# Kernel optimization log

Measured on AMD Instinct MI355X. Metric: run time of the kernel, lower is better.

The kernel has to match this reference:

```python
import jax, jax.numpy as jnp
import numpy as np

N = 100000   # nodes
E = 1600000  # edges
G = 512      # graphs
EPS_MSG = 1e-7   # GENConv message eps
EPS_SM = 1e-16   # PyG softmax denom eps
BN_EPS = 1e-5    # BatchNorm eps (eval mode, running mean=0, var=1)


def setup_inputs() -> dict:
    key = jax.random.key(0)
    ks = iter(jax.random.split(key, 40))
    d = {}
    d['x'] = jax.random.normal(next(ks), (N, 10), dtype=jnp.float32)
    d['edge_index'] = jax.random.randint(next(ks), (2, E), 0, N, dtype=jnp.int64)
    d['batch'] = jax.random.randint(next(ks), (N,), 0, G, dtype=jnp.int64)

    def lin(k, fo, fi):
        k1, k2 = jax.random.split(k)
        s = 1.0 / np.sqrt(fi)
        return (jax.random.uniform(k1, (fo, fi), jnp.float32, -s, s),
                jax.random.uniform(k2, (fo,), jnp.float32, -s, s))

    # conv1: lin_src/lin_dst 10->100, MLP [100,200,100] with BN(200)
    d['c1_src_w'], d['c1_src_b'] = lin(next(ks), 100, 10)
    d['c1_dst_w'], d['c1_dst_b'] = lin(next(ks), 100, 10)
    d['c1_w1'], d['c1_b1'] = lin(next(ks), 200, 100)
    d['c1_g'] = jnp.ones((200,), jnp.float32)
    d['c1_be'] = jnp.zeros((200,), jnp.float32)
    d['c1_w2'], d['c1_b2'] = lin(next(ks), 100, 200)
    # conv2 / conv3: in==out -> no lin_src/dst; MLP [100,200,100]
    for p in ('c2', 'c3'):
        d[p + '_w1'], d[p + '_b1'] = lin(next(ks), 200, 100)
        d[p + '_g'] = jnp.ones((200,), jnp.float32)
        d[p + '_be'] = jnp.zeros((200,), jnp.float32)
        d[p + '_w2'], d[p + '_b2'] = lin(next(ks), 100, 200)
    d['fc1_w'], d['fc1_b'] = lin(next(ks), 100, 200)
    d['cls_w'], d['cls_b'] = lin(next(ks), 2, 100)
    return d


def _genconv(x, src, dst, src_w, src_b, dst_w, dst_b, w1, b1, g, be, w2, b2):
    # GENConv, aggr='softmax', t=1, eval-mode BN in MLP
    h = x if src_w is None else x @ src_w.T + src_b          # [N, 100]
    msg = jax.nn.relu(h[src]) + EPS_MSG                       # [E, 100]
    m = jax.ops.segment_max(msg, dst, num_segments=N)
    m = jnp.where(jnp.isfinite(m), m, 0.0)
    e = jnp.exp(msg - m[dst])
    den = jax.ops.segment_sum(e, dst, num_segments=N)
    alpha = e / (den[dst] + EPS_SM)
    agg = jax.ops.segment_sum(alpha * msg, dst, num_segments=N)  # [N, 100]
    xd = x if dst_w is None else x @ dst_w.T + dst_b
    out = agg + xd
    # MLP: Linear -> BN(eval: mean0,var1) -> ReLU -> Linear
    hh = out @ w1.T + b1
    hh = hh * (g / np.sqrt(1.0 + BN_EPS)) + be
    hh = jax.nn.relu(hh)
    return hh @ w2.T + b2


def _readout(x, batch):
    s = jax.ops.segment_sum(x, batch, num_segments=G)
    cnt = jax.ops.segment_sum(jnp.ones((x.shape[0],), x.dtype), batch, num_segments=G)
    mean = s / jnp.maximum(cnt, 1.0)[:, None]
    mx = jax.ops.segment_max(x, batch, num_segments=G)
    mx = jnp.where(jnp.isfinite(mx), mx, 0.0)
    return jnp.concatenate([mean, mx], axis=-1)  # [G, 200]


def reference(x, edge_index, batch,
              c1_src_w, c1_src_b, c1_dst_w, c1_dst_b, c1_w1, c1_b1, c1_g, c1_be, c1_w2, c1_b2,
              c2_w1, c2_b1, c2_g, c2_be, c2_w2, c2_b2,
              c3_w1, c3_b1, c3_g, c3_be, c3_w2, c3_b2,
              fc1_w, fc1_b, cls_w, cls_b):
    src, dst = edge_index[0], edge_index[1]
    h = jax.nn.relu(_genconv(x, src, dst, c1_src_w, c1_src_b, c1_dst_w, c1_dst_b,
                             c1_w1, c1_b1, c1_g, c1_be, c1_w2, c1_b2))
    x1 = _readout(h, batch)
    h = jax.nn.relu(_genconv(h, src, dst, None, None, None, None,
                             c2_w1, c2_b1, c2_g, c2_be, c2_w2, c2_b2))
    x2 = _readout(h, batch)
    h = jax.nn.relu(_genconv(h, src, dst, None, None, None, None,
                             c3_w1, c3_b1, c3_g, c3_be, c3_w2, c3_b2))
    x3 = _readout(h, batch)
    encode = jax.nn.relu(x1) + jax.nn.relu(x2) + jax.nn.relu(x3)  # [G, 200]
    z = jax.nn.relu(encode @ fc1_w.T + fc1_b)  # dropout is identity in eval
    logits = z @ cls_w.T + cls_b               # [G, 2]
    return (logits, encode)
```

## Files before the change

### kernel.cpp

```cpp
#include <hip/hip_runtime.h>
#include <cstdint>
#include <cstddef>

#define XF 10
#define NF 100
#define HF 200
#define BSHIFT 8
#define NBLK_G 512
#define MAXBK 512
#define RCH 4

typedef _Float16 f16x8 __attribute__((ext_vector_type(8)));
typedef _Float16 h2 __attribute__((ext_vector_type(2)));
typedef float f32x4 __attribute__((ext_vector_type(4)));

static __device__ __forceinline__ float bn_scale(float g) {
    return g * 0.9999950000374997f;
}

__global__ __launch_bounds__(256) void csr_count_kernel(const int* __restrict__ eidx,
                                                        int* __restrict__ bmat,
                                                        int E, int nbk, int epb) {
    __shared__ int hist[MAXBK];
    for (int j = threadIdx.x; j < nbk; j += 256) hist[j] = 0;
    __syncthreads();
    int base = blockIdx.x * epb;
    int end = base + epb; if (end > E) end = E;
    for (int e = base + threadIdx.x; e < end; e += 256) {
        int d = eidx[E + e];
        atomicAdd(&hist[d >> BSHIFT], 1);
    }
    __syncthreads();
    for (int j = threadIdx.x; j < nbk; j += 256)
        bmat[(size_t)j * NBLK_G + blockIdx.x] = hist[j];
}

__global__ __launch_bounds__(256) void scan1x_kernel(int* __restrict__ a,
                                                     int* __restrict__ blocksum, int n) {
    __shared__ int s[256];
    int t = threadIdx.x;
    int base = blockIdx.x * 1024 + t * 4;
    int v[4]; int tot = 0;
#pragma unroll
    for (int i = 0; i < 4; ++i) {
        v[i] = (base + i < n) ? a[base + i] : 0;
        tot += v[i];
    }
    s[t] = tot;
    __syncthreads();
    for (int off = 1; off < 256; off <<= 1) {
        int add = (t >= off) ? s[t - off] : 0;
        __syncthreads();
        s[t] += add;
        __syncthreads();
    }
    int run = s[t] - tot;
#pragma unroll
    for (int i = 0; i < 4; ++i) {
        if (base + i < n) a[base + i] = run;
        run += v[i];
    }
    if (t == 255) blocksum[blockIdx.x] = s[255];
}

__global__ void small_scan_kernel(const int* __restrict__ in, int in_stride,
                                  int* __restrict__ cur, int cur_stride,
                                  int* __restrict__ indptr, int n) {
    __shared__ int s[256];
    int t = threadIdx.x;
    int base = t * 4;
    int v[4]; int tot = 0;
#pragma unroll
    for (int i = 0; i < 4; ++i) {
        v[i] = (base + i < n) ? in[(base + i) * in_stride] : 0;
        tot += v[i];
    }
    s[t] = tot;
    __syncthreads();
    for (int off = 1; off < 256; off <<= 1) {
        int add = (t >= off) ? s[t - off] : 0;
        __syncthreads();
        s[t] += add;
        __syncthreads();
    }
    int run = s[t] - tot;
#pragma unroll
    for (int i = 0; i < 4; ++i) {
        if (base + i < n) {
            cur[(base + i) * cur_stride] = run;
            run += v[i];
            if (indptr) indptr[base + i + 1] = run;
        }
    }
    if (t == 0 && indptr) indptr[0] = 0;
}

__global__ __launch_bounds__(256) void csr_scatter_kernel(const int* __restrict__ eidx,
                                                          const int* __restrict__ bmat,
                                                          const int* __restrict__ blocksum,
                                                          int* __restrict__ packed,
                                                          int E, int nbk, int epb) {
    __shared__ int cur[MAXBK];
    for (int j = threadIdx.x; j < nbk; j += 256) {
        size_t idx = (size_t)j * NBLK_G + blockIdx.x;
        cur[j] = bmat[idx] + blocksum[idx >> 10];
    }
    __syncthreads();
    int base = blockIdx.x * epb;
    int end = base + epb; if (end > E) end = E;
    for (int e = base + threadIdx.x; e < end; e += 256) {
        int s = eidx[e];
        int d = eidx[E + e];
        int p = atomicAdd(&cur[d >> BSHIFT], 1);
        packed[p] = s | ((d & 255) << 24);
    }
}

__global__ __launch_bounds__(256) void csr_finalize_kernel(const int* __restrict__ bmat,
                                                           const int* __restrict__ blocksum,
                                                           const int* __restrict__ packed,
                                                           int* __restrict__ indptr,
                                                           int* __restrict__ esrc,
                                                           int E, int nbk, int n) {
    __shared__ int cnt[256];
    __shared__ int s[256];
    __shared__ int cur[256];
    int b = blockIdx.x;
    int t = threadIdx.x;
    size_t i0 = (size_t)b * NBLK_G;
    int ebeg = bmat[i0] + blocksum[i0 >> 10];
    int eend = E;
    if (b + 1 < nbk) {
        size_t i1 = (size_t)(b + 1) * NBLK_G;
        eend = bmat[i1] + blocksum[i1 >> 10];
    }
    cnt[t] = 0;
    __syncthreads();
    for (int i = ebeg + t; i < eend; i += 256)
        atomicAdd(&cnt[((unsigned)packed[i]) >> 24], 1);
    __syncthreads();
    int tot = cnt[t];
    s[t] = tot;
    __syncthreads();
    for (int off = 1; off < 256; off <<= 1) {
        int add = (t >= off) ? s[t - off] : 0;
        __syncthreads();
        s[t] += add;
        __syncthreads();
    }
    int off_ex = s[t] - tot;
    int node = (b << BSHIFT) + t;
    if (node < n) indptr[node] = ebeg + off_ex;
    if (b == nbk - 1 && t == 0) indptr[n] = E;
    cur[t] = ebeg + off_ex;
    __syncthreads();
    for (int i = ebeg + t; i < eend; i += 256) {
        int p = packed[i];
        int pos = atomicAdd(&cur[((unsigned)p) >> 24], 1);
        esrc[pos] = p & 0xFFFFFF;
    }
}

__global__ __launch_bounds__(256) void gcnt_kernel(const int* __restrict__ batch,
                                                   int* __restrict__ gcount, int n) {
    int i = blockIdx.x * 256 + threadIdx.x;
    if (i < n) atomicAdd(&gcount[batch[i]], 1);
}

__global__ __launch_bounds__(256) void gfill_kernel(const int* __restrict__ batch,
                                                    int* __restrict__ gcur,
                                                    int* __restrict__ gnodes, int n) {
    int i = blockIdx.x * 256 + threadIdx.x;
    if (i >= n) return;
    int g = batch[i];
    int p = atomicAdd(&gcur[g], 1);
    gnodes[p] = i;
}

struct WArgs {
    const float* src[6];
    _Float16* dst[6];
};
__global__ __launch_bounds__(256) void wconv_kernel(WArgs wa) {
    int w = blockIdx.y;
    int idx = blockIdx.x * 256 + threadIdx.x;
    int J, K, j, k;
    if (w < 3) { J = 200; K = 100; j = idx >> 7; k = idx & 127; }
    else       { J = 100; K = 200; j = idx >> 8; k = idx & 255; }
    float v = (j < J && k < K) ? wa.src[w][j * K + k] : 0.f;
    wa.dst[w][idx] = (_Float16)v;
}

__global__ __launch_bounds__(256) void lin10_kernel(const float* __restrict__ x,
                                                    const float* __restrict__ sw,
                                                    const float* __restrict__ sb,
                                                    const float* __restrict__ dw,
                                                    const float* __restrict__ db,
                                                    _Float16* __restrict__ h16,
                                                    _Float16* __restrict__ xd16, int n_nodes) {
    int t = threadIdx.x;
    int slot = t >> 6, lane = t & 63;
    bool act = lane < 50;
    int f0 = 2 * lane, f1 = f0 + 1;
    float ws0[XF], ws1[XF], wd0[XF], wd1[XF];
    float bs0 = 0.f, bs1 = 0.f, bd0 = 0.f, bd1 = 0.f;
    if (act) {
#pragma unroll
        for (int k = 0; k < XF; ++k) {
            ws0[k] = sw[f0 * XF + k]; ws1[k] = sw[f1 * XF + k];
            wd0[k] = dw[f0 * XF + k]; wd1[k] = dw[f1 * XF + k];
        }
        bs0 = sb[f0]; bs1 = sb[f1]; bd0 = db[f0]; bd1 = db[f1];
    }
    for (int it = 0; it < 16; ++it) {
        int n = blockIdx.x * 64 + it * 4 + slot;
        if (n >= n_nodes) continue;
        float a0 = bs0, a1 = bs1, b0 = bd0, b1 = bd1;
        if (act) {
            const float2* xp = (const float2*)(x + (size_t)n * XF);
            float xv[XF];
#pragma unroll
            for (int k = 0; k < 5; ++k) { float2 v = xp[k]; xv[2 * k] = v.x; xv[2 * k + 1] = v.y; }
#pragma unroll
            for (int k = 0; k < XF; ++k) {
                a0 = fmaf(xv[k], ws0[k], a0);
                a1 = fmaf(xv[k], ws1[k], a1);
                b0 = fmaf(xv[k], wd0[k], b0);
                b1 = fmaf(xv[k], wd1[k], b1);
            }
        } else { a0 = a1 = b0 = b1 = 0.f; }
        ((h2*)(h16 + (size_t)n * 128))[lane] = (h2){(_Float16)a0, (_Float16)a1};
        ((h2*)(xd16 + (size_t)n * 128))[lane] = (h2){(_Float16)b0, (_Float16)b1};
    }
}

__global__ __launch_bounds__(128) void agg_kernel(const _Float16* __restrict__ h16,
                                                  const _Float16* __restrict__ xd16,
                                                  const int* __restrict__ indptr,
                                                  const int* __restrict__ esrc,
                                                  _Float16* __restrict__ c16, int n_nodes) {
    int n = blockIdx.x * 2 + (threadIdx.x >> 6);
    if (n >= n_nodes) return;
    int lane = threadIdx.x & 63;
    int ln = (lane < 50) ? lane : 0;
    int beg = __builtin_amdgcn_readfirstlane(indptr[n]);
    int end = __builtin_amdgcn_readfirstlane(indptr[n + 1]);
    int deg = end - beg;
    const h2* hb = (const h2*)h16;
    float d0 = 0.f, d1 = 0.f, s0 = 0.f, s1 = 0.f;
    const float L2E = 1.44269504088896f;
    h2 va[8], vb[8];
    if (deg > 0) {
#pragma unroll
        for (int k = 0; k < 8; ++k) {
            int j = (k < deg) ? k : deg - 1;
            unsigned sidx = (unsigned)esrc[beg + j];
            va[k] = hb[(size_t)sidx * 64 + ln];
        }
    }
    for (int r = 0; r < deg; r += 8) {
        if (r + 8 < deg) {
#pragma unroll
            for (int k = 0; k < 8; ++k) {
                int j = (r + 8 + k < deg) ? r + 8 + k : deg - 1;
                unsigned sidx = (unsigned)esrc[beg + j];
                vb[k] = hb[(size_t)sidx * 64 + ln];
            }
        }
        int km = deg - r; if (km > 8) km = 8;
#pragma unroll
        for (int k = 0; k < 8; ++k) {
            if (k < km) {
                float a0 = fmaxf((float)va[k].x, 0.f) + 1e-7f;
                float a1 = fmaxf((float)va[k].y, 0.f) + 1e-7f;
                float e0 = __builtin_amdgcn_exp2f(fmaf(a0, L2E, -40.f));
                float e1 = __builtin_amdgcn_exp2f(fmaf(a1, L2E, -40.f));
                d0 += e0; s0 = fmaf(e0, a0, s0);
                d1 += e1; s1 = fmaf(e1, a1, s1);
            }
        }
#pragma unroll
        for (int k = 0; k < 8; ++k) va[k] = vb[k];
    }
    const float EPS = 9.094947e-29f;
    float g0 = s0 / (d0 + EPS);
    float g1 = s1 / (d1 + EPS);
    float o0 = 0.f, o1 = 0.f;
    if (lane < 50) {
        h2 xv = ((const h2*)(xd16 + (size_t)n * 128))[lane];
        o0 = g0 + (float)xv.x;
        o1 = g1 + (float)xv.y;
    }
    ((h2*)(c16 + (size_t)n * 128))[lane] = (h2){(_Float16)o0, (_Float16)o1};
}

__global__ __launch_bounds__(256, 3) void mlp_fused_kernel(const _Float16* __restrict__ A,
                                                           const _Float16* __restrict__ W1,
                                                           const float* __restrict__ b1v,
                                                           const float* __restrict__ g1v,
                                                           const float* __restrict__ be1v,
                                                           const _Float16* __restrict__ W2,
                                                           const float* __restrict__ b2v,
                                                           _Float16* __restrict__ out16,
                                                           int M) {
    __shared__ _Float16 hh[64][264];
    int wave = threadIdx.x >> 6;
    int lane = threadIdx.x & 63;
    int l15 = lane & 15, quad = lane >> 4;
    long m0 = (long)blockIdx.x * 64;

    const _Float16* aptr = A + (m0 + l15) * 128 + quad * 8;
    const _Float16* w1p  = W1 + (size_t)(wave * 64 + l15) * 128 + quad * 8;
    f32x4 acc[4][4] = {};
#pragma unroll 2
    for (int ks = 0; ks < 4; ++ks) {
        f16x8 bfr[4], afr[4];
#pragma unroll
        for (int ct = 0; ct < 4; ++ct) bfr[ct] = *(const f16x8*)(w1p + (size_t)ct * 16 * 128 + ks * 32);
#pragma unroll
        for (int i = 0; i < 4; ++i) afr[i] = *(const f16x8*)(aptr + (size_t)i * 16 * 128 + ks * 32);
#pragma unroll
        for (int i = 0; i < 4; ++i)
#pragma unroll
            for (int ct = 0; ct < 4; ++ct)
                acc[i][ct] = __builtin_amdgcn_mfma_f32_16x16x32_f16(afr[i], bfr[ct], acc[i][ct], 0, 0, 0);
    }
#pragma unroll
    for (int ct = 0; ct < 4; ++ct) {
        int col = wave * 64 + ct * 16 + l15;
        bool cv = col < HF;
        float bi = cv ? b1v[col] : 0.f;
        float gm = cv ? bn_scale(g1v[col]) : 0.f;
        float bt = cv ? be1v[col] : 0.f;
#pragma unroll
        for (int i = 0; i < 4; ++i)
#pragma unroll
            for (int r = 0; r < 4; ++r) {
                float v = fmaxf((acc[i][ct][r] + bi) * gm + bt, 0.f);
                hh[i * 16 + quad * 4 + r][col] = (_Float16)v;
            }
    }
    __syncthreads();

    const _Float16* w2p = W2 + (size_t)(wave * 32 + l15) * 256 + quad * 8;
    f32x4 o[4][2] = {};
#pragma unroll 2
    for (int ks = 0; ks < 8; ++ks) {
        f16x8 bfr[2], afr[4];
#pragma unroll
        for (int ct = 0; ct < 2; ++ct) bfr[ct] = *(const f16x8*)(w2p + (size_t)ct * 16 * 256 + ks * 32);
#pragma unroll
        for (int i = 0; i < 4; ++i) afr[i] = *(const f16x8*)(&hh[i * 16 + l15][quad * 8 + ks * 32]);
#pragma unroll
        for (int i = 0; i < 4; ++i)
#pragma unroll
            for (int ct = 0; ct < 2; ++ct)
                o[i][ct] = __builtin_amdgcn_mfma_f32_16x16x32_f16(afr[i], bfr[ct], o[i][ct], 0, 0, 0);
    }
#pragma unroll
    for (int ct = 0; ct < 2; ++ct) {
        int col = wave * 32 + ct * 16 + l15;
        bool cv = col < NF;
        float bi = cv ? b2v[col] : 0.f;
#pragma unroll
        for (int i = 0; i < 4; ++i)
#pragma unroll
            for (int r = 0; r < 4; ++r) {
                long row = m0 + i * 16 + quad * 4 + r;
                float v = fmaxf(o[i][ct][r] + bi, 0.f);
                if (!cv) v = 0.f;
                if (row < M) out16[row * 128 + col] = (_Float16)v;
            }
    }
}

__global__ __launch_bounds__(256) void readout2_kernel(const _Float16* __restrict__ h16,
                                                       const int* __restrict__ gindptr,
                                                       const int* __restrict__ gnodes,
                                                       float* __restrict__ sumpart,
                                                       float* __restrict__ maxpart, int G) {
    __shared__ float ls[4][128];
    __shared__ float lm[4][128];
    int g = blockIdx.x, ch = blockIdx.y;
    int wave = threadIdx.x >> 6;
    int lane = threadIdx.x & 63;
    int ln = (lane < 50) ? lane : 0;
    int beg = gindptr[g], end = gindptr[g + 1];
    const h2* hb = (const h2*)h16;
    float s0 = 0.f, s1 = 0.f, m0 = 0.f, m1 = 0.f;
    int i = beg + ch * 4 + wave;
    int nd = (i < end) ? gnodes[i] : 0;
    for (; i < end; i += 16) {
        int ndn = (i + 16 < end) ? gnodes[i + 16] : 0;
        h2 v = hb[(size_t)nd * 64 + ln];
        float v0 = (float)v.x, v1 = (float)v.y;
        s0 += v0; s1 += v1;
        m0 = fmaxf(m0, v0); m1 = fmaxf(m1, v1);
        nd = ndn;
    }
    ls[wave][2 * lane] = s0; ls[wave][2 * lane + 1] = s1;
    lm[wave][2 * lane] = m0; lm[wave][2 * lane + 1] = m1;
    __syncthreads();
    int f = threadIdx.x;
    if (f < NF) {
        float ss = ls[0][f] + ls[1][f] + ls[2][f] + ls[3][f];
        float mm = fmaxf(fmaxf(lm[0][f], lm[1][f]), fmaxf(lm[2][f], lm[3][f]));
        sumpart[((size_t)ch * G + g) * NF + f] = ss;
        maxpart[((size_t)ch * G + g) * NF + f] = mm;
    }
}

__global__ __launch_bounds__(256) void head_kernel(const float* __restrict__ rbuf,
                                                   const int* __restrict__ gindptr,
                                                   const float* __restrict__ fc1w,
                                                   const float* __restrict__ fc1b,
                                                   const float* __restrict__ clsw,
                                                   const float* __restrict__ clsb,
                                                   float* __restrict__ out, int G) {
    __shared__ float enc[HF];
    __shared__ float z[NF];
    int g = blockIdx.x;
    int t = threadIdx.x;
    float ic = 1.f / fmaxf((float)(gindptr[g + 1] - gindptr[g]), 1.f);
    if (t < HF) {
        float e = 0.f;
        if (t < NF) {
#pragma unroll
            for (int l = 0; l < 3; ++l) {
                float s = 0.f;
#pragma unroll
                for (int ch = 0; ch < RCH; ++ch)
                    s += rbuf[(((size_t)(l * 2) * RCH + ch) * G + g) * NF + t];
                e += fmaxf(s * ic, 0.f);
            }
        } else {
            int f = t - NF;
#pragma unroll
            for (int l = 0; l < 3; ++l) {
                float mm = 0.f;
#pragma unroll
                for (int ch = 0; ch < RCH; ++ch)
                    mm = fmaxf(mm, rbuf[(((size_t)(l * 2 + 1) * RCH + ch) * G + g) * NF + f]);
                e += fmaxf(mm, 0.f);
            }
        }
        enc[t] = e;
        out[G * 2 + (size_t)g * HF + t] = e;
    }
    __syncthreads();
    if (t < NF) {
        float a = fc1b[t];
        for (int k = 0; k < HF; ++k) a += enc[k] * fc1w[t * HF + k];
        z[t] = fmaxf(a, 0.f);
    }
    __syncthreads();
    if (t < 2) {
        float a = clsb[t];
        for (int k = 0; k < NF; ++k) a += z[k] * clsw[t * NF + k];
        out[(size_t)g * 2 + t] = a;
    }
}

extern "C" void kernel_launch(void* const* d_in, const int* in_sizes, int n_in,
                              void* d_out, int out_size, void* d_ws, size_t ws_size,
                              hipStream_t stream) {
    const float* x        = (const float*)d_in[0];
    const int*   eidx     = (const int*)d_in[1];
    const int*   batch    = (const int*)d_in[2];
    const float* c1_src_w = (const float*)d_in[3];
    const float* c1_src_b = (const float*)d_in[4];
    const float* c1_dst_w = (const float*)d_in[5];
    const float* c1_dst_b = (const float*)d_in[6];
    const float* cw1[3] = {(const float*)d_in[7],  (const float*)d_in[13], (const float*)d_in[19]};
    const float* cb1[3] = {(const float*)d_in[8],  (const float*)d_in[14], (const float*)d_in[20]};
    const float* cg[3]  = {(const float*)d_in[9],  (const float*)d_in[15], (const float*)d_in[21]};
    const float* cbe[3] = {(const float*)d_in[10], (const float*)d_in[16], (const float*)d_in[22]};
    const float* cw2[3] = {(const float*)d_in[11], (const float*)d_in[17], (const float*)d_in[23]};
    const float* cb2[3] = {(const float*)d_in[12], (const float*)d_in[18], (const float*)d_in[24]};
    const float* fc1w = (const float*)d_in[25];
    const float* fc1b = (const float*)d_in[26];
    const float* clsw = (const float*)d_in[27];
    const float* clsb = (const float*)d_in[28];

    const int N = in_sizes[0] / XF;
    const int E = in_sizes[1] / 2;
    const int G = out_size / 202;
    const int Mpad = (N + 63) & ~63;
    const int NBK = (N + 255) >> BSHIFT;
    const int EPB = (E + NBLK_G - 1) / NBLK_G;
    const int BM = NBK * NBLK_G;
    const int NB2 = (BM + 1023) / 1024;

    char* p = (char*)d_ws;
    auto alloc = [&](size_t bytes) {
        char* r = p;
        p += (bytes + 255) & ~(size_t)255;
        return r;
    };
    _Float16* h16  = (_Float16*)alloc((size_t)Mpad * 128 * 2);
    _Float16* C16  = (_Float16*)alloc((size_t)Mpad * 128 * 2);
    _Float16* xd16 = (_Float16*)alloc((size_t)Mpad * 128 * 2);
    _Float16* W16  = (_Float16*)alloc((size_t)6 * 32768 * 2);
    int* packed   = (int*)alloc((size_t)E * 4);
    int* esrc     = (int*)alloc((size_t)E * 4);
    int* indptr   = (int*)alloc((size_t)(N + 1) * 4);
    int* bmat     = (int*)alloc((size_t)BM * 4);
    int* blocksum = (int*)alloc((size_t)NB2 * 4);
    int* gcount   = (int*)alloc((size_t)G * 4);
    int* gcur     = (int*)alloc((size_t)G * 4);
    int* gindptr  = (int*)alloc((size_t)(G + 1) * 4);
    int* gnodes   = (int*)alloc((size_t)N * 4);
    float* rbuf   = (float*)alloc((size_t)6 * RCH * G * NF * 4);

    (void)hipMemsetAsync(gcount, 0, (size_t)G * 4, stream);

    csr_count_kernel<<<NBLK_G, 256, 0, stream>>>(eidx, bmat, E, NBK, EPB);
    scan1x_kernel<<<NB2, 256, 0, stream>>>(bmat, blocksum, BM);
    small_scan_kernel<<<1, 256, 0, stream>>>(blocksum, 1, blocksum, 1, nullptr, NB2);
    csr_scatter_kernel<<<NBLK_G, 256, 0, stream>>>(eidx, bmat, blocksum, packed, E, NBK, EPB);
    csr_finalize_kernel<<<NBK, 256, 0, stream>>>(bmat, blocksum, packed, indptr, esrc, E, NBK, N);

    gcnt_kernel<<<(N + 255) / 256, 256, 0, stream>>>(batch, gcount, N);
    small_scan_kernel<<<1, 256, 0, stream>>>(gcount, 1, gcur, 1, gindptr, G);
    gfill_kernel<<<(N + 255) / 256, 256, 0, stream>>>(batch, gcur, gnodes, N);

    WArgs wa;
    for (int l = 0; l < 3; ++l) {
        wa.src[l] = cw1[l];     wa.dst[l] = W16 + (size_t)l * 32768;
        wa.src[3 + l] = cw2[l]; wa.dst[3 + l] = W16 + (size_t)(3 + l) * 32768;
    }
    wconv_kernel<<<dim3(128, 6), 256, 0, stream>>>(wa);

    lin10_kernel<<<(N + 63) / 64, 256, 0, stream>>>(x, c1_src_w, c1_src_b,
                                                    c1_dst_w, c1_dst_b, h16, xd16, N);

    for (int l = 0; l < 3; ++l) {
        const _Float16* xdp = (l == 0) ? xd16 : h16;
        agg_kernel<<<(N + 1) / 2, 128, 0, stream>>>(h16, xdp, indptr, esrc, C16, N);
        mlp_fused_kernel<<<Mpad / 64, 256, 0, stream>>>(
            C16, W16 + (size_t)l * 32768, cb1[l], cg[l], cbe[l],
            W16 + (size_t)(3 + l) * 32768, cb2[l], h16, N);
        readout2_kernel<<<dim3(G, RCH), 256, 0, stream>>>(
            h16, gindptr, gnodes,
            rbuf + (size_t)(l * 2) * RCH * G * NF,
            rbuf + (size_t)(l * 2 + 1) * RCH * G * NF, G);
    }

    head_kernel<<<G, 256, 0, stream>>>(rbuf, gindptr, fc1w, fc1b, clsw, clsb, (float*)d_out, G);
    (void)ws_size;
}
```

Before: 635.3 us.

## Split each node's edge aggregation across two waves and skip redundant ReLU

The aggregation kernel now gives each destination node two wavefronts, each handling alternating edges, and merges their partial softmax sums through shared memory before the final divide and residual add. This doubles the memory-level parallelism per node for the gather-heavy edge loop, which has an average degree of 16. A template flag also drops the ReLU in layers 2 and 3, whose inputs already passed through a ReLU. The cost is a block-wide barrier and an LDS exchange, plus a second wave sitting idle during the finalize step.

New measurement: 865.2 us. 36.2% more time.

```diff
diff --git a/kernel.cpp b/kernel.cpp
--- a/kernel.cpp
+++ b/kernel.cpp
@@ -234,64 +234,79 @@
     }
 }
 
-__global__ __launch_bounds__(128) void agg_kernel(const _Float16* __restrict__ h16,
+template <bool RELU>
+__global__ __launch_bounds__(256) void agg_kernel(const _Float16* __restrict__ h16,
                                                   const _Float16* __restrict__ xd16,
                                                   const int* __restrict__ indptr,
                                                   const int* __restrict__ esrc,
                                                   _Float16* __restrict__ c16, int n_nodes) {
-    int n = blockIdx.x * 2 + (threadIdx.x >> 6);
-    if (n >= n_nodes) return;
+    __shared__ float4 part[4][64];
+    int wave = threadIdx.x >> 6;
     int lane = threadIdx.x & 63;
+    int half = wave & 1;
+    int n = blockIdx.x * 2 + (wave >> 1);
     int ln = (lane < 50) ? lane : 0;
-    int beg = __builtin_amdgcn_readfirstlane(indptr[n]);
-    int end = __builtin_amdgcn_readfirstlane(indptr[n + 1]);
-    int deg = end - beg;
     const h2* hb = (const h2*)h16;
+    const float L2E = 1.44269504088896f;
     float d0 = 0.f, d1 = 0.f, s0 = 0.f, s1 = 0.f;
-    const float L2E = 1.44269504088896f;
-    h2 va[8], vb[8];
-    if (deg > 0) {
-#pragma unroll
-        for (int k = 0; k < 8; ++k) {
-            int j = (k < deg) ? k : deg - 1;
-            unsigned sidx = (unsigned)esrc[beg + j];
-            va[k] = hb[(size_t)sidx * 64 + ln];
+    if (n < n_nodes) {
+        int beg = __builtin_amdgcn_readfirstlane(indptr[n]);
+        int end = __builtin_amdgcn_readfirstlane(indptr[n + 1]);
+        int deg = end - beg;
+        int cnt = (deg - half + 1) >> 1;
+        if (cnt > 0) {
+            int base = beg + half;
+            h2 va[8], vb[8];
+#pragma unroll
+            for (int k = 0; k < 8; ++k) {
+                int j = (k < cnt) ? k : cnt - 1;
+                unsigned sidx = (unsigned)esrc[base + 2 * j];
+                va[k] = hb[(size_t)sidx * 64 + ln];
+            }
+            for (int r = 0; r < cnt; r += 8) {
+                if (r + 8 < cnt) {
+#pragma unroll
+                    for (int k = 0; k < 8; ++k) {
+                        int j = (r + 8 + k < cnt) ? r + 8 + k : cnt - 1;
+                        unsigned sidx = (unsigned)esrc[base + 2 * j];
+                        vb[k] = hb[(size_t)sidx * 64 + ln];
+                    }
+                }
+                int km = cnt - r; if (km > 8) km = 8;
+#pragma unroll
+                for (int k = 0; k < 8; ++k) {
+                    if (k < km) {
+                        float a0 = (float)va[k].x;
+                        float a1 = (float)va[k].y;
+                        if (RELU) { a0 = fmaxf(a0, 0.f); a1 = fmaxf(a1, 0.f); }
+                        a0 += 1e-7f; a1 += 1e-7f;
+                        float e0 = __builtin_amdgcn_exp2f(fmaf(a0, L2E, -40.f));
+                        float e1 = __builtin_amdgcn_exp2f(fmaf(a1, L2E, -40.f));
+                        d0 += e0; s0 = fmaf(e0, a0, s0);
+                        d1 += e1; s1 = fmaf(e1, a1, s1);
+                    }
+                }
+#pragma unroll
+                for (int k = 0; k < 8; ++k) va[k] = vb[k];
+            }
         }
     }
-    for (int r = 0; r < deg; r += 8) {
-        if (r + 8 < deg) {
-#pragma unroll
-            for (int k = 0; k < 8; ++k) {
-                int j = (r + 8 + k < deg) ? r + 8 + k : deg - 1;
-                unsigned sidx = (unsigned)esrc[beg + j];
-                vb[k] = hb[(size_t)sidx * 64 + ln];
-            }
+    part[wave][lane] = make_float4(d0, d1, s0, s1);
+    __syncthreads();
+    if (half == 0 && n < n_nodes) {
+        float4 o = part[wave | 1][lane];
+        d0 += o.x; d1 += o.y; s0 += o.z; s1 += o.w;
+        const float EPS = 9.094947e-29f;
+        float g0 = s0 / (d0 + EPS);
+        float g1 = s1 / (d1 + EPS);
+        float o0 = 0.f, o1 = 0.f;
+        if (lane < 50) {
+            h2 xv = ((const h2*)(xd16 + (size_t)n * 128))[lane];
+            o0 = g0 + (float)xv.x;
+            o1 = g1 + (float)xv.y;
         }
-        int km = deg - r; if (km > 8) km = 8;
-#pragma unroll
-        for (int k = 0; k < 8; ++k) {
-            if (k < km) {
-                float a0 = fmaxf((float)va[k].x, 0.f) + 1e-7f;
-                float a1 = fmaxf((float)va[k].y, 0.f) + 1e-7f;
-                float e0 = __builtin_amdgcn_exp2f(fmaf(a0, L2E, -40.f));
-                float e1 = __builtin_amdgcn_exp2f(fmaf(a1, L2E, -40.f));
-                d0 += e0; s0 = fmaf(e0, a0, s0);
-                d1 += e1; s1 = fmaf(e1, a1, s1);
-            }
-        }
-#pragma unroll
-        for (int k = 0; k < 8; ++k) va[k] = vb[k];
-    }
-    const float EPS = 9.094947e-29f;
-    float g0 = s0 / (d0 + EPS);
-    float g1 = s1 / (d1 + EPS);
-    float o0 = 0.f, o1 = 0.f;
-    if (lane < 50) {
-        h2 xv = ((const h2*)(xd16 + (size_t)n * 128))[lane];
-        o0 = g0 + (float)xv.x;
-        o1 = g1 + (float)xv.y;
-    }
-    ((h2*)(c16 + (size_t)n * 128))[lane] = (h2){(_Float16)o0, (_Float16)o1};
+        ((h2*)(c16 + (size_t)n * 128))[lane] = (h2){(_Float16)o0, (_Float16)o1};
+    }
 }
 
 __global__ __launch_bounds__(256, 3) void mlp_fused_kernel(const _Float16* __restrict__ A,
@@ -536,7 +551,10 @@
 
     for (int l = 0; l < 3; ++l) {
         const _Float16* xdp = (l == 0) ? xd16 : h16;
-        agg_kernel<<<(N + 1) / 2, 128, 0, stream>>>(h16, xdp, indptr, esrc, C16, N);
+        if (l == 0)
+            agg_kernel<true><<<(N + 1) / 2, 256, 0, stream>>>(h16, xdp, indptr, esrc, C16, N);
+        else
+            agg_kernel<false><<<(N + 1) / 2, 256, 0, stream>>>(h16, xdp, indptr, esrc, C16, N);
         mlp_fused_kernel<<<Mpad / 64, 256, 0, stream>>>(
             C16, W16 + (size_t)l * 32768, cb1[l], cg[l], cbe[l],
             W16 + (size_t)(3 + l) * 32768, cb2[l], h16, N);
```
